# Kernel optimization log

Hardware: AMD Instinct MI355X
Metric: run time of the kernel (lower is better)

## Reference

```python
import jax, jax.numpy as jnp
import numpy as np

B, NUM_ROIS, NUM_GT = 32, 8192, 128
NUM_SAMPLED = 512
POS_FRAC = 0.25
BACKGROUND = 0.0
VARIANCE = np.array([0.1, 0.1, 0.2, 0.2], np.float32)  # [dy, dx, dh, dw]
IMG = 1024.0


def _make_boxes(key, shape):
    # valid yxyx boxes: positive height/width, inside image
    kc, ks = jax.random.split(key)
    c = jax.random.uniform(kc, shape[:-1] + (2,), minval=0.2, maxval=0.8) * IMG
    hw = jax.random.uniform(ks, shape[:-1] + (2,), minval=0.05, maxval=0.3) * IMG
    return jnp.concatenate([c - 0.5 * hw, c + 0.5 * hw], axis=-1)


def setup_inputs() -> dict:
    key = jax.random.key(0)
    k1, k2, k3, k4 = jax.random.split(key, 4)
    rois = _make_boxes(k1, (B, NUM_ROIS, 4))
    gt_boxes = _make_boxes(k2, (B, NUM_GT, 4))
    gt_classes = jax.random.randint(k3, (B, NUM_GT, 1), 1, 81).astype(jnp.float32)
    # uniform noise used by balanced_sample (channel 0 for positives, 1 for negatives)
    sample_noise = jax.random.uniform(k4, (B, NUM_ROIS + NUM_GT, 2), dtype=jnp.float32)
    return {"rois": rois, "gt_boxes": gt_boxes, "gt_classes": gt_classes,
            "sample_noise": sample_noise}


def _compute_iou(a, b):
    # a: [B,N,4], b: [B,G,4] in yxyx; use_masking=True -> padded (-1) boxes get iou=-1
    a_ = a[:, :, None, :]   # [B,N,1,4]
    b_ = b[:, None, :, :]   # [B,1,G,4]
    iy = jnp.maximum(jnp.minimum(a_[..., 2], b_[..., 2]) - jnp.maximum(a_[..., 0], b_[..., 0]), 0.0)
    ix = jnp.maximum(jnp.minimum(a_[..., 3], b_[..., 3]) - jnp.maximum(a_[..., 1], b_[..., 1]), 0.0)
    inter = iy * ix
    area_a = (a[..., 2] - a[..., 0]) * (a[..., 3] - a[..., 1])  # [B,N]
    area_b = (b[..., 2] - b[..., 0]) * (b[..., 3] - b[..., 1])  # [B,G]
    union = area_a[:, :, None] + area_b[:, None, :] - inter
    iou = inter / jnp.maximum(union, 1e-8)
    mask_a = jnp.all(a == -1.0, axis=-1)  # [B,N] padded rois
    mask_b = jnp.all(b == -1.0, axis=-1)  # [B,G] padded gt
    masked = mask_a[:, :, None] | mask_b[:, None, :]
    return jnp.where(masked, -1.0, iou)


def _encode_deltas(anchors, boxes):
    # yxyx -> (dy,dx,dh,dw)/variance
    ah = anchors[..., 2] - anchors[..., 0]
    aw = anchors[..., 3] - anchors[..., 1]
    acy = anchors[..., 0] + 0.5 * ah
    acx = anchors[..., 1] + 0.5 * aw
    bh = boxes[..., 2] - boxes[..., 0]
    bw = boxes[..., 3] - boxes[..., 1]
    bcy = boxes[..., 0] + 0.5 * bh
    bcx = boxes[..., 1] + 0.5 * bw
    d = jnp.stack([(bcy - acy) / ah, (bcx - acx) / aw,
                   jnp.log(bh / ah), jnp.log(bw / aw)], axis=-1)
    return d / jnp.asarray(VARIANCE, d.dtype)


def _balanced_sample(pos, neg, noise, num_samples, pos_frac):
    # returns float indicator [B,N]: 1.0 for sampled rois
    num_pos = int(num_samples * pos_frac)
    num_neg = num_samples - num_pos
    b, n = pos.shape
    pos_scores = jnp.where(pos, noise[..., 0], -1.0)
    neg_scores = jnp.where(neg, noise[..., 1], -1.0)
    _, pi = jax.lax.top_k(pos_scores, num_pos)
    _, ni = jax.lax.top_k(neg_scores, num_neg)
    rows = jnp.arange(b)[:, None]
    # only mark picks that are actually positive/negative (handles scarcity)
    pv = jnp.take_along_axis(pos, pi, axis=-1).astype(jnp.float32)
    nv = jnp.take_along_axis(neg, ni, axis=-1).astype(jnp.float32)
    ind = jnp.zeros((b, n), jnp.float32)
    ind = ind.at[rows, pi].add(pv)
    ind = ind.at[rows, ni].add(nv)  # pos/neg disjoint -> stays in {0,1}
    return ind


def _gather(t, idx):
    # t: [B,M,D], idx: [B,K] -> [B,K,D]
    return jnp.take_along_axis(t, idx[..., None], axis=1)


def reference(rois, gt_boxes, gt_classes, sample_noise):
    # append_gt_boxes=True
    rois_all = jnp.concatenate([rois, gt_boxes], axis=1)  # [B, N+G, 4]
    sim = _compute_iou(rois_all, gt_boxes)                # [B, N+G, G]
    matched_cols = jnp.argmax(sim, axis=-1)               # [B, N+G]
    max_iou = jnp.max(sim, axis=-1)
    # ArgmaxBoxMatcher(thresholds=[0.0,0.5], match_values=[-2,-1,1])
    matched_vals = jnp.where(max_iou >= 0.5, 1, jnp.where(max_iou >= 0.0, -1, -2))
    positive = matched_vals == 1
    negative = matched_vals == -1
    background = ~positive                                # [B, N+G]

    matched_gt_classes = _gather(gt_classes, matched_cols)
    matched_gt_classes = jnp.where(background[..., None], BACKGROUND, matched_gt_classes)
    matched_gt_boxes = _gather(gt_boxes, matched_cols)
    encoded = _encode_deltas(rois_all, matched_gt_boxes)
    encoded = jnp.where(background[..., None], 0.0, encoded)

    indicators = _balanced_sample(positive, negative, sample_noise, NUM_SAMPLED, POS_FRAC)
    sampled_indicators, sampled_idx = jax.lax.top_k(indicators, NUM_SAMPLED)

    sampled_rois = _gather(rois_all, sampled_idx)
    sampled_gt_boxes = _gather(encoded, sampled_idx)
    sampled_gt_classes = _gather(matched_gt_classes, sampled_idx)
    sampled_box_weights = _gather(positive[..., None].astype(gt_boxes.dtype), sampled_idx)
    sampled_class_weights = sampled_indicators[..., None].astype(gt_classes.dtype)
    return (sampled_rois, sampled_gt_boxes, sampled_box_weights,
            sampled_gt_classes, sampled_class_weights)
```

## Files before the change

### kernel.cpp

```cpp
#include <hip/hip_runtime.h>
#include <cstdint>

#define NB 32
#define NROIS 8192
#define NGT 128
#define NALL (NROIS + NGT)
#define NSAMP 512
#define KPOS 128
#define KNEG 384
#define BCAP 1024
#define TS 1024
#define CH 9
#define JC 4
#define JL 16

template <bool MASKED>
__device__ __forceinline__ void match_half(
    const float4* __restrict__ sg, const float* __restrict__ sab,
    const unsigned char* __restrict__ smk,
    const int half, const float4 A, const float aar, const bool ma,
    float* best, int* bcol)
{
  #pragma clang fp contract(off)
  const int jb = half * 64;
  #pragma unroll 4
  for (int jj = 0; jj < JL; ++jj) {
    #pragma unroll
    for (int c = 0; c < JC; ++c) {
      const int j = jb + c * JL + jj;
      const float4 g = sg[j];
      const float ab = sab[j];
      float iy = fmaxf(fminf(A.z, g.z) - fmaxf(A.x, g.x), 0.0f);
      float ix = fmaxf(fminf(A.w, g.w) - fmaxf(A.y, g.y), 0.0f);
      float inter = iy * ix;
      float uni = (aar + ab) - inter;
      float iou = inter / fmaxf(uni, 1e-8f);
      if (MASKED) { if (ma || (smk[j] != 0)) iou = -1.0f; }
      if (iou > best[c]) { best[c] = iou; bcol[c] = j; }
    }
  }
}

__global__ __launch_bounds__(256) void k_match(
    const float* __restrict__ rois,
    const float* __restrict__ gt,
    const float* __restrict__ noise,
    int* __restrict__ mword)
{
  #pragma clang fp contract(off)
  __shared__ float4 sg[NGT];
  __shared__ float sab[NGT];
  __shared__ unsigned char smk[NGT];
  __shared__ int s_anymask;
  __shared__ float mbest[128];
  __shared__ int mcol[128];

  const int b = blockIdx.y;
  const int tid = threadIdx.x;

  bool mflag = false;
  if (tid < NGT) {
    float4 g = reinterpret_cast<const float4*>(gt)[b * NGT + tid];
    sg[tid] = g;
    sab[tid] = (g.z - g.x) * (g.w - g.y);
    mflag = (g.x == -1.0f) && (g.y == -1.0f) && (g.z == -1.0f) && (g.w == -1.0f);
    smk[tid] = mflag;
  }
  if (tid == 0) s_anymask = 0;
  __syncthreads();
  if (mflag) atomicOr(&s_anymask, 1);
  __syncthreads();

  const int r = tid & 127;
  const int half = tid >> 7;
  const int i = blockIdx.x * 128 + r;

  float4 A = (i < NROIS)
    ? reinterpret_cast<const float4*>(rois)[b * NROIS + i]
    : sg[i - NROIS];
  const float aar = (A.z - A.x) * (A.w - A.y);
  const bool ma = (A.x == -1.0f) && (A.y == -1.0f) && (A.z == -1.0f) && (A.w == -1.0f);

  float best[JC];
  int bcol[JC];
  #pragma unroll
  for (int c = 0; c < JC; ++c) { best[c] = -3.0e38f; bcol[c] = half * 64 + c * JL; }

  if (s_anymask == 0 && __ballot(ma) == 0ULL) {
    match_half<false>(sg, sab, smk, half, A, aar, ma, best, bcol);
  } else {
    match_half<true>(sg, sab, smk, half, A, aar, ma, best, bcol);
  }

  float bb = best[0];
  int cc = bcol[0];
  #pragma unroll
  for (int c = 1; c < JC; ++c) {
    if (best[c] > bb) { bb = best[c]; cc = bcol[c]; }
  }

  if (half) { mbest[r] = bb; mcol[r] = cc; }
  __syncthreads();
  if (!half) {
    const float b1 = mbest[r];
    if (b1 > bb) { bb = b1; cc = mcol[r]; }
    const int code = (bb >= 0.5f) ? 3 : ((bb >= 0.0f) ? 1 : 0);
    float2 nz = reinterpret_cast<const float2*>(noise)[b * NALL + i];
    float v = (code == 3) ? nz.x : nz.y;
    int bin = (int)(v * 1024.0f);
    bin = bin < 0 ? 0 : (bin > 1023 ? 1023 : bin);
    mword[b * NALL + i] = cc | (code << 7) | (bin << 9);
  }
}

__device__ __forceinline__ int block_incl_scan(int v, int tid, int* wsum) {
  __syncthreads();
  int s = v;
  #pragma unroll
  for (int off = 1; off < 64; off <<= 1) {
    int u = __shfl_up(s, off);
    if ((tid & 63) >= off) s += u;
  }
  const int wid = tid >> 6;
  if ((tid & 63) == 63) wsum[wid] = s;
  __syncthreads();
  if (wid == 0) {
    const int lane = tid & 63;
    int w = (lane < (TS >> 6)) ? wsum[lane] : 0;
    #pragma unroll
    for (int off = 1; off < (TS >> 6); off <<= 1) {
      int u = __shfl_up(w, off);
      if (lane >= off) w += u;
    }
    if (lane < (TS >> 6)) wsum[lane] = w;
  }
  __syncthreads();
  return s + (wid ? wsum[wid - 1] : 0);
}

__global__ __launch_bounds__(TS) void k_select(
    const int* __restrict__ mword,
    const float* __restrict__ noise,
    const float* __restrict__ rois,
    const float* __restrict__ gt,
    const float* __restrict__ gtcls,
    float* __restrict__ out)
{
  #pragma clang fp contract(off)
  const int b = blockIdx.x;
  const int tid = threadIdx.x;

  __shared__ int hist[1024];
  __shared__ int wsum[TS >> 6];
  __shared__ int s_total;
  __shared__ float bval[2][BCAP];
  __shared__ int bidx_[2][BCAP];
  __shared__ int bcnt[2];
  __shared__ int s_bstar[2], s_need[2];
  __shared__ unsigned char ind[NALL];
  __shared__ unsigned short sorder[NSAMP];

  int ew[CH];

  hist[tid] = 0;
  if (tid < 2) bcnt[tid] = 0;

  #pragma unroll
  for (int k = 0; k < CH; ++k) {
    const int i = tid + k * TS;
    int w = 0;
    if (i < NALL) {
      ind[i] = 0;
      w = mword[b * NALL + i];
    }
    ew[k] = w;
  }
  __syncthreads();
  #pragma unroll
  for (int k = 0; k < CH; ++k) {
    const int w = ew[k];
    if (w & 0x80) atomicAdd(&hist[w >> 9], (w & 0x100) ? 1 : (1 << 16));
  }
  __syncthreads();

  const int c = hist[tid];
  const int incl = block_incl_scan(c, tid, wsum);
  if (tid == TS - 1) s_total = incl;
  __syncthreads();
  const int total = s_total;

  #pragma unroll
  for (int p = 0; p < 2; ++p) {
    const int want = p ? KNEG : KPOS;
    const int sh = p ? 16 : 0;
    const int tot = (total >> sh) & 0xFFFF;
    if (tot >= want) {
      const int inc = (incl >> sh) & 0xFFFF;
      const int cp = (c >> sh) & 0xFFFF;
      const int above = tot - inc;
      if (above < want && above + cp >= want) {
        s_bstar[p] = tid; s_need[p] = want - above;
      }
    }
  }
  __syncthreads();

  const bool selall0 = ((total & 0xFFFF) < KPOS);
  const bool selall1 = (((total >> 16) & 0xFFFF) < KNEG);

  #pragma unroll
  for (int k = 0; k < CH; ++k) {
    const int w = ew[k];
    if (w & 0x80) {
      const int i = tid + k * TS;
      const int p = (w & 0x100) ? 0 : 1;
      const bool selall = p ? selall1 : selall0;
      const int bin = w >> 9;
      if (selall || bin > s_bstar[p]) {
        ind[i] = 1;
      } else if (bin == s_bstar[p]) {
        int pos = atomicAdd(&bcnt[p], 1);
        if (pos < BCAP) {
          bval[p][pos] = noise[((size_t)(b * NALL + i)) * 2 + p];
          bidx_[p][pos] = i;
        }
      }
    }
  }
  __syncthreads();

  #pragma unroll
  for (int p = 0; p < 2; ++p) {
    const bool selall = p ? selall1 : selall0;
    if (selall) continue;
    int cnt = bcnt[p]; if (cnt > BCAP) cnt = BCAP;
    const int need = s_need[p];
    for (int x = tid; x < cnt; x += TS) {
      const float v = bval[p][x];
      const int id = bidx_[p][x];
      int rank = 0;
      for (int y = 0; y < cnt; ++y) {
        const float vy = bval[p][y];
        const int iy2 = bidx_[p][y];
        rank += (vy > v) || (vy == v && iy2 < id);
      }
      if (rank < need) ind[id] = 1;
    }
  }
  __syncthreads();

  const int start = tid * CH;
  const int end = (start + CH < NALL) ? (start + CH) : NALL;
  int cnt1 = 0;
  for (int i = start; i < end; ++i) cnt1 += ind[i];
  const int incl1 = block_incl_scan(cnt1, tid, wsum);
  if (tid == TS - 1) s_total = incl1;
  __syncthreads();
  const int K1 = s_total;
  int ones_before = incl1 - cnt1;
  const int nzero = NSAMP - K1;
  for (int i = start; i < end; ++i) {
    if (ind[i]) {
      sorder[ones_before] = (unsigned short)i;
      ones_before++;
    } else {
      const int zrank = i - ones_before;
      if (zrank < nzero) sorder[K1 + zrank] = (unsigned short)i;
    }
  }
  __syncthreads();

  if (tid < NSAMP) {
    const int s = tid;
    const int idx = sorder[s];
    const size_t t = (size_t)b * NSAMP + s;

    float4 A = (idx < NROIS)
      ? reinterpret_cast<const float4*>(rois)[b * NROIS + idx]
      : reinterpret_cast<const float4*>(gt)[b * NGT + (idx - NROIS)];

    const int w = mword[b * NALL + idx];
    const int col = w & 0x7F;
    const bool pos = (((w >> 7) & 3) == 3);

    float e0 = 0.f, e1 = 0.f, e2 = 0.f, e3 = 0.f, cls = 0.f;
    if (pos) {
      float4 G = reinterpret_cast<const float4*>(gt)[b * NGT + col];
      float ah = A.z - A.x, aw = A.w - A.y;
      float acy = A.x + 0.5f * ah, acx = A.y + 0.5f * aw;
      float bh = G.z - G.x, bw = G.w - G.y;
      float bcy = G.x + 0.5f * bh, bcx = G.y + 0.5f * bw;
      e0 = ((bcy - acy) / ah) / 0.1f;
      e1 = ((bcx - acx) / aw) / 0.1f;
      e2 = logf(bh / ah) / 0.2f;
      e3 = logf(bw / aw) / 0.2f;
      cls = gtcls[b * NGT + col];
    }

    float* o_rois = out;
    float* o_enc  = out + (size_t)NB * NSAMP * 4;
    float* o_bw   = out + (size_t)NB * NSAMP * 8;
    float* o_cls  = o_bw + (size_t)NB * NSAMP;
    float* o_cw   = o_cls + (size_t)NB * NSAMP;

    reinterpret_cast<float4*>(o_rois)[t] = A;
    float4 E; E.x = e0; E.y = e1; E.z = e2; E.w = e3;
    reinterpret_cast<float4*>(o_enc)[t] = E;
    o_bw[t]  = pos ? 1.0f : 0.0f;
    o_cls[t] = cls;
    o_cw[t]  = (s < K1) ? 1.0f : 0.0f;
  }
}

extern "C" void kernel_launch(void* const* d_in, const int* in_sizes, int n_in,
                              void* d_out, int out_size, void* d_ws, size_t ws_size,
                              hipStream_t stream) {
  const float* rois  = (const float*)d_in[0];
  const float* gt    = (const float*)d_in[1];
  const float* gtcls = (const float*)d_in[2];
  const float* noise = (const float*)d_in[3];
  float* out = (float*)d_out;

  int* mword = (int*)d_ws;

  dim3 g1(NALL / 128, NB);
  k_match<<<g1, 256, 0, stream>>>(rois, gt, noise, mword);
  k_select<<<NB, TS, 0, stream>>>(mword, noise, rois, gt, gtcls, out);
}
```

Before: 44.66 us.

## Load GT boxes via scalar loads and give each thread a full ROI

The match kernel now uses 128 threads per block, and each thread scans all 128 GT boxes for one ROI. This removes the two-half split and the shared-memory merge between halves. GT boxes are read into scalar registers with inline s_load_dwordx16 asm rather than staged as float4 in LDS, and only GT areas stay in LDS. Each scalar load is followed by an immediate waitcnt, so load latency is serialized. Fewer threads per block also lowers per-block parallelism, and the masked fallback path is rewritten as a simple loop.

```diff
diff --git a/kernel.cpp b/kernel.cpp
--- a/kernel.cpp
+++ b/kernel.cpp
@@ -11,106 +11,117 @@
 #define BCAP 1024
 #define TS 1024
 #define CH 9
-#define JC 4
-#define JL 16
-
-template <bool MASKED>
-__device__ __forceinline__ void match_half(
-    const float4* __restrict__ sg, const float* __restrict__ sab,
-    const unsigned char* __restrict__ smk,
-    const int half, const float4 A, const float aar, const bool ma,
-    float* best, int* bcol)
+
+typedef float f32x16 __attribute__((ext_vector_type(16)));
+
+template <int N>
+__device__ __forceinline__ void octet(
+    const float* __restrict__ gptr, const float* __restrict__ sab,
+    const float4 A, const float aar, float* best, int* bcol)
 {
   #pragma clang fp contract(off)
-  const int jb = half * 64;
-  #pragma unroll 4
-  for (int jj = 0; jj < JL; ++jj) {
-    #pragma unroll
-    for (int c = 0; c < JC; ++c) {
-      const int j = jb + c * JL + jj;
-      const float4 g = sg[j];
-      const float ab = sab[j];
-      float iy = fmaxf(fminf(A.z, g.z) - fmaxf(A.x, g.x), 0.0f);
-      float ix = fmaxf(fminf(A.w, g.w) - fmaxf(A.y, g.y), 0.0f);
-      float inter = iy * ix;
-      float uni = (aar + ab) - inter;
-      float iou = inter / fmaxf(uni, 1e-8f);
-      if (MASKED) { if (ma || (smk[j] != 0)) iou = -1.0f; }
-      if (iou > best[c]) { best[c] = iou; bcol[c] = j; }
-    }
-  }
-}
-
-__global__ __launch_bounds__(256) void k_match(
+  f32x16 g0, g1;
+  asm volatile("s_load_dwordx16 %0, %1, %2\n\ts_waitcnt lgkmcnt(0)"
+               : "=&s"(g0) : "s"(gptr), "i"(N * 128));
+  asm volatile("s_load_dwordx16 %0, %1, %2\n\ts_waitcnt lgkmcnt(0)"
+               : "=&s"(g1) : "s"(gptr), "i"(N * 128 + 64));
+  #pragma unroll
+  for (int k = 0; k < 8; ++k) {
+    const int j = N * 8 + k;
+    const float gx = (k < 4) ? g0[4 * k + 0] : g1[4 * (k - 4) + 0];
+    const float gy = (k < 4) ? g0[4 * k + 1] : g1[4 * (k - 4) + 1];
+    const float gz = (k < 4) ? g0[4 * k + 2] : g1[4 * (k - 4) + 2];
+    const float gw = (k < 4) ? g0[4 * k + 3] : g1[4 * (k - 4) + 3];
+    const float ab = sab[j];
+    float iy = fmaxf(fminf(A.z, gz) - fmaxf(A.x, gx), 0.0f);
+    float ix = fmaxf(fminf(A.w, gw) - fmaxf(A.y, gy), 0.0f);
+    float inter = iy * ix;
+    float uni = (aar + ab) - inter;
+    float iou = inter / fmaxf(uni, 1e-8f);
+    const int c = j & 3;
+    if (iou > best[c]) { best[c] = iou; bcol[c] = j; }
+  }
+}
+
+__global__ __launch_bounds__(128) void k_match(
     const float* __restrict__ rois,
     const float* __restrict__ gt,
     const float* __restrict__ noise,
     int* __restrict__ mword)
 {
   #pragma clang fp contract(off)
-  __shared__ float4 sg[NGT];
   __shared__ float sab[NGT];
-  __shared__ unsigned char smk[NGT];
-  __shared__ int s_anymask;
-  __shared__ float mbest[128];
-  __shared__ int mcol[128];
+  __shared__ unsigned long long smask[2];
 
   const int b = blockIdx.y;
   const int tid = threadIdx.x;
-
-  bool mflag = false;
-  if (tid < NGT) {
-    float4 g = reinterpret_cast<const float4*>(gt)[b * NGT + tid];
-    sg[tid] = g;
-    sab[tid] = (g.z - g.x) * (g.w - g.y);
-    mflag = (g.x == -1.0f) && (g.y == -1.0f) && (g.z == -1.0f) && (g.w == -1.0f);
-    smk[tid] = mflag;
-  }
-  if (tid == 0) s_anymask = 0;
-  __syncthreads();
-  if (mflag) atomicOr(&s_anymask, 1);
-  __syncthreads();
-
-  const int r = tid & 127;
-  const int half = tid >> 7;
-  const int i = blockIdx.x * 128 + r;
-
-  float4 A = (i < NROIS)
-    ? reinterpret_cast<const float4*>(rois)[b * NROIS + i]
-    : sg[i - NROIS];
+  const float4* gt4 = reinterpret_cast<const float4*>(gt) + (size_t)b * NGT;
+  const float* gptr = gt + (size_t)b * NGT * 4;
+
+  float4 g = gt4[tid];
+  sab[tid] = (g.z - g.x) * (g.w - g.y);
+  const bool mflag = (g.x == -1.0f) && (g.y == -1.0f) && (g.z == -1.0f) && (g.w == -1.0f);
+  const unsigned long long mb = __ballot(mflag);
+  if ((tid & 63) == 0) smask[tid >> 6] = mb;
+  __syncthreads();
+  const bool anymask = (smask[0] | smask[1]) != 0ULL;
+
+  const int i = blockIdx.x * 128 + tid;
+  float4 A = (blockIdx.x < 64)
+    ? (reinterpret_cast<const float4*>(rois) + (size_t)b * NROIS)[i]
+    : gt4[tid];
   const float aar = (A.z - A.x) * (A.w - A.y);
   const bool ma = (A.x == -1.0f) && (A.y == -1.0f) && (A.z == -1.0f) && (A.w == -1.0f);
 
-  float best[JC];
-  int bcol[JC];
-  #pragma unroll
-  for (int c = 0; c < JC; ++c) { best[c] = -3.0e38f; bcol[c] = half * 64 + c * JL; }
-
-  if (s_anymask == 0 && __ballot(ma) == 0ULL) {
-    match_half<false>(sg, sab, smk, half, A, aar, ma, best, bcol);
+  float bb;
+  int cc;
+  if (!anymask && __ballot(ma) == 0ULL) {
+    float best[4];
+    int bcol[4];
+    #pragma unroll
+    for (int c = 0; c < 4; ++c) { best[c] = -3.0e38f; bcol[c] = c; }
+    octet<0>(gptr, sab, A, aar, best, bcol);
+    octet<1>(gptr, sab, A, aar, best, bcol);
+    octet<2>(gptr, sab, A, aar, best, bcol);
+    octet<3>(gptr, sab, A, aar, best, bcol);
+    octet<4>(gptr, sab, A, aar, best, bcol);
+    octet<5>(gptr, sab, A, aar, best, bcol);
+    octet<6>(gptr, sab, A, aar, best, bcol);
+    octet<7>(gptr, sab, A, aar, best, bcol);
+    octet<8>(gptr, sab, A, aar, best, bcol);
+    octet<9>(gptr, sab, A, aar, best, bcol);
+    octet<10>(gptr, sab, A, aar, best, bcol);
+    octet<11>(gptr, sab, A, aar, best, bcol);
+    octet<12>(gptr, sab, A, aar, best, bcol);
+    octet<13>(gptr, sab, A, aar, best, bcol);
+    octet<14>(gptr, sab, A, aar, best, bcol);
+    octet<15>(gptr, sab, A, aar, best, bcol);
+    bb = best[0]; cc = bcol[0];
+    #pragma unroll
+    for (int c = 1; c < 4; ++c) {
+      if (best[c] > bb || (best[c] == bb && bcol[c] < cc)) { bb = best[c]; cc = bcol[c]; }
+    }
   } else {
-    match_half<true>(sg, sab, smk, half, A, aar, ma, best, bcol);
-  }
-
-  float bb = best[0];
-  int cc = bcol[0];
-  #pragma unroll
-  for (int c = 1; c < JC; ++c) {
-    if (best[c] > bb) { bb = best[c]; cc = bcol[c]; }
-  }
-
-  if (half) { mbest[r] = bb; mcol[r] = cc; }
-  __syncthreads();
-  if (!half) {
-    const float b1 = mbest[r];
-    if (b1 > bb) { bb = b1; cc = mcol[r]; }
-    const int code = (bb >= 0.5f) ? 3 : ((bb >= 0.0f) ? 1 : 0);
-    float2 nz = reinterpret_cast<const float2*>(noise)[b * NALL + i];
-    float v = (code == 3) ? nz.x : nz.y;
-    int bin = (int)(v * 1024.0f);
-    bin = bin < 0 ? 0 : (bin > 1023 ? 1023 : bin);
-    mword[b * NALL + i] = cc | (code << 7) | (bin << 9);
-  }
+    bb = -3.0e38f; cc = 0;
+    for (int j = 0; j < NGT; ++j) {
+      float4 gg = gt4[j];
+      const bool mj = (gg.x == -1.0f) && (gg.y == -1.0f) && (gg.z == -1.0f) && (gg.w == -1.0f);
+      float iy = fmaxf(fminf(A.z, gg.z) - fmaxf(A.x, gg.x), 0.0f);
+      float ix = fmaxf(fminf(A.w, gg.w) - fmaxf(A.y, gg.y), 0.0f);
+      float inter = iy * ix;
+      float uni = (aar + sab[j]) - inter;
+      float iou = inter / fmaxf(uni, 1e-8f);
+      if (ma || mj) iou = -1.0f;
+      if (iou > bb) { bb = iou; cc = j; }
+    }
+  }
+
+  const int code = (bb >= 0.5f) ? 3 : ((bb >= 0.0f) ? 1 : 0);
+  float2 nz = reinterpret_cast<const float2*>(noise)[(size_t)b * NALL + i];
+  float v = (code == 3) ? nz.x : nz.y;
+  int bin = (int)(v * 1024.0f);
+  bin = bin < 0 ? 0 : (bin > 1023 ? 1023 : bin);
+  mword[(size_t)b * NALL + i] = cc | (code << 7) | (bin << 9);
 }
 
 __device__ __forceinline__ int block_incl_scan(int v, int tid, int* wsum) {
@@ -171,7 +182,7 @@
     int w = 0;
     if (i < NALL) {
       ind[i] = 0;
-      w = mword[b * NALL + i];
+      w = mword[(size_t)b * NALL + i];
     }
     ew[k] = w;
   }
@@ -221,7 +232,7 @@
       } else if (bin == s_bstar[p]) {
         int pos = atomicAdd(&bcnt[p], 1);
         if (pos < BCAP) {
-          bval[p][pos] = noise[((size_t)(b * NALL + i)) * 2 + p];
+          bval[p][pos] = noise[((size_t)b * NALL + i) * 2 + p];
           bidx_[p][pos] = i;
         }
       }
@@ -276,16 +287,16 @@
     const size_t t = (size_t)b * NSAMP + s;
 
     float4 A = (idx < NROIS)
-      ? reinterpret_cast<const float4*>(rois)[b * NROIS + idx]
-      : reinterpret_cast<const float4*>(gt)[b * NGT + (idx - NROIS)];
-
-    const int w = mword[b * NALL + idx];
+      ? reinterpret_cast<const float4*>(rois)[(size_t)b * NROIS + idx]
+      : reinterpret_cast<const float4*>(gt)[(size_t)b * NGT + (idx - NROIS)];
+
+    const int w = mword[(size_t)b * NALL + idx];
     const int col = w & 0x7F;
     const bool pos = (((w >> 7) & 3) == 3);
 
     float e0 = 0.f, e1 = 0.f, e2 = 0.f, e3 = 0.f, cls = 0.f;
     if (pos) {
-      float4 G = reinterpret_cast<const float4*>(gt)[b * NGT + col];
+      float4 G = reinterpret_cast<const float4*>(gt)[(size_t)b * NGT + col];
       float ah = A.z - A.x, aw = A.w - A.y;
       float acy = A.x + 0.5f * ah, acx = A.y + 0.5f * aw;
       float bh = G.z - G.x, bw = G.w - G.y;
@@ -294,7 +305,7 @@
       e1 = ((bcx - acx) / aw) / 0.1f;
       e2 = logf(bh / ah) / 0.2f;
       e3 = logf(bw / aw) / 0.2f;
-      cls = gtcls[b * NGT + col];
+      cls = gtcls[(size_t)b * NGT + col];
     }
 
     float* o_rois = out;
@@ -324,6 +335,6 @@
   int* mword = (int*)d_ws;
 
   dim3 g1(NALL / 128, NB);
-  k_match<<<g1, 256, 0, stream>>>(rois, gt, noise, mword);
+  k_match<<<g1, 128, 0, stream>>>(rois, gt, noise, mword);
   k_select<<<NB, TS, 0, stream>>>(mword, noise, rois, gt, gtcls, out);
 }
```

New measurement: 50.23 us. +12.5%, slower.
